# Optimization experiments

Measured on AMD Instinct MI355X. Metric: run time of the kernel, lower is better.

## Reference

```python
import jax, jax.numpy as jnp
import numpy as np

B, P, CD, V = 4096, 64, 2, 3
D, K, H, L, S, NI, NF = 128, 2048, 256, 5, 4, 100000, 10
COMMIT = 0.25
IN_DIM = CD + CD * 2 * NF  # 42


def _lin(k, out, inn):
    kw, kb = jax.random.split(k)
    lim = 1.0 / np.sqrt(inn)
    W = jax.random.uniform(kw, (out, inn), jnp.float32, -lim, lim)
    b = jax.random.uniform(kb, (out,), jnp.float32, -lim, lim)
    return W, b


def setup_inputs() -> dict:
    key = jax.random.key(0)
    ks = jax.random.split(key, 8)
    coords = jax.random.uniform(ks[0], (B, P, CD), jnp.float32) * 2.0 - 1.0
    latent_indices = jax.random.randint(ks[1], (B,), 0, NI)
    latents = jax.random.normal(ks[2], (NI, S, D), jnp.float32)
    emb = jax.random.normal(ks[3], (S, K, D), jnp.float32)
    vq_emb = emb / jnp.linalg.norm(emb, axis=-1, keepdims=True)
    mod = [_lin(jax.random.fold_in(ks[4], i), H, D) for i in range(L)]
    mod_W = jnp.stack([w for w, _ in mod])
    mod_b = jnp.stack([b for _, b in mod])
    dec_W0, dec_b0 = _lin(ks[5], H, IN_DIM)
    hid = [_lin(jax.random.fold_in(ks[6], i), H, H) for i in range(L - 1)]
    dec_Wh = jnp.stack([w for w, _ in hid])
    dec_bh = jnp.stack([b for _, b in hid])
    last_W, last_b = _lin(ks[7], V, H)
    return dict(coords=coords, latent_indices=latent_indices, latents=latents,
                vq_emb=vq_emb, mod_W=mod_W, mod_b=mod_b,
                dec_W0=dec_W0, dec_b0=dec_b0, dec_Wh=dec_Wh, dec_bh=dec_bh,
                last_W=last_W, last_b=last_b)


def reference(coords, latent_indices, latents, vq_emb, mod_W, mod_b,
              dec_W0, dec_b0, dec_Wh, dec_bh, last_W, last_b):
    sg = jax.lax.stop_gradient
    img_lat = latents[latent_indices]  # (B, S, D) gather from large table
    z_q_sum = jnp.zeros((B, D), coords.dtype)
    residual = jnp.zeros((B, D), coords.dtype)
    total_vq_loss = jnp.zeros((), coords.dtype)
    for s in range(S):  # sequential residual VQ stages (structural, S=4)
        z_stage = img_lat[:, s, :]
        if s == 0:
            residual = z_stage
            z_cur = z_stage
        else:
            residual = residual + z_stage
            z_cur = residual - sg(z_q_sum)
        emb = vq_emb[s]  # (K, D)
        # squared distances via expansion: ||z||^2 - 2 z e^T + ||e||^2
        dists = (jnp.sum(z_cur * z_cur, axis=1, keepdims=True)
                 - 2.0 * z_cur @ emb.T
                 + jnp.sum(emb * emb, axis=1))  # (B, K)
        idx = jnp.argmin(dists, axis=1)  # (B,)
        z_q = emb[idx]  # (B, D) codebook gather
        z_q_st = z_cur + sg(z_q - z_cur)  # straight-through
        total_vq_loss = total_vq_loss + COMMIT * jnp.mean((sg(z_q) - z_cur) ** 2)
        z_q_sum = z_q_sum + z_q_st
    # FiLM betas: (L, B, H)
    betas = jnp.einsum('lhd,bd->lbh', mod_W, z_q_sum) + mod_b[:, None, :]
    # positional encoding: concat[x, sin(x*2^f*pi), cos(x*2^f*pi)]
    freqs = (2.0 ** jnp.arange(NF, dtype=coords.dtype)) * np.pi  # (NF,)
    xe = coords[..., None] * freqs  # (B, P, CD, NF)
    enc = jnp.concatenate([coords,
                           jnp.sin(xe).reshape(B, P, -1),
                           jnp.cos(xe).reshape(B, P, -1)], axis=-1)  # (B,P,42)
    x = jax.nn.relu(jnp.einsum('bpi,hi->bph', enc, dec_W0) + dec_b0
                    + betas[0][:, None, :])
    for i in range(1, L):
        x = jax.nn.relu(jnp.einsum('bph,gh->bpg', x, dec_Wh[i - 1]) + dec_bh[i - 1]
                        + betas[i][:, None, :])
    values = jnp.einsum('bph,vh->bpv', x, last_W) + last_b  # (B, P, V)
    return values, total_vq_loss
```

## Files before the change

### kernel.cpp

```cpp
#include <hip/hip_runtime.h>

typedef unsigned short u16;
typedef unsigned int u32;
typedef __attribute__((ext_vector_type(8))) short short8;
typedef __attribute__((ext_vector_type(4))) float f32x4;

__device__ __forceinline__ float b2f(u16 u) {
    return __builtin_bit_cast(float, (u32)u << 16);
}
__device__ __forceinline__ u16 f2b(float f) {
    u32 x = __builtin_bit_cast(u32, f);
    x += 0x7fffu + ((x >> 16) & 1u);
    return (u16)(x >> 16);
}

#define WS_LPART  0
#define WS_ENORM  512
#define WS_ZQSUM  8704
#define WS_BETAS  532992
#define WS_W0PAD  3154432
#define WS_DWH    3162624
#define WS_VQH    WS_BETAS
#define WS_VQL    (WS_BETAS + 524288)

__global__ __launch_bounds__(64) void enorm_kernel(const float* __restrict__ vq,
                                                   float* __restrict__ enorm) {
    int code = blockIdx.x;
    int lane = threadIdx.x;
    const float* e = vq + (size_t)code * 128;
    float a = e[lane], b = e[lane + 64];
    float v = a * a + b * b;
    #pragma unroll
    for (int off = 32; off; off >>= 1) v += __shfl_down(v, off);
    if (lane == 0) enorm[code] = v;
}

__global__ __launch_bounds__(256) void vqsplit_kernel(const float* __restrict__ vq,
                                                      u16* __restrict__ vh,
                                                      u16* __restrict__ vl) {
    int i = blockIdx.x * 256 + threadIdx.x;
    float v = vq[i];
    u16 h = f2b(v);
    vh[i] = h;
    vl[i] = f2b(v - b2f(h));
}

__global__ __launch_bounds__(256) void padw0_kernel(const float* __restrict__ W0,
                                                    u16* __restrict__ w0pad) {
    int i = blockIdx.x * 256 + threadIdx.x;
    int row = i >> 6, k = i & 63;
    w0pad[i] = (k < 42) ? f2b(W0[row * 42 + k]) : (u16)0;
}

__global__ __launch_bounds__(256) void dwh_kernel(const float* __restrict__ Wh,
                                                  u16* __restrict__ dwh) {
    int i = blockIdx.x * 256 + threadIdx.x;
    dwh[i] = f2b(Wh[i]);
}

__global__ __launch_bounds__(512, 2) void vq_kernel(const int* __restrict__ lidx,
                                                    const float* __restrict__ latents,
                                                    const float* __restrict__ vq,
                                                    const u16* __restrict__ vqh,
                                                    const u16* __restrict__ vql,
                                                    const float* __restrict__ enorm,
                                                    float* __restrict__ zqsum_g,
                                                    float* __restrict__ lpartial) {
    int tid = threadIdx.x;
    int wv = tid >> 6;
    int lane = tid & 63;
    int col = lane & 15;
    int g = lane >> 4;
    int urow = tid >> 5;
    int uc = tid & 31;

    __shared__ __align__(16) float s_resid[16][132];
    __shared__ __align__(16) float s_zqsum[16][132];
    __shared__ __align__(16) float s_zcur[16][132];
    __shared__ float rd1[32][16], rd2[32][16];
    __shared__ int   ri1[32][16], ri2[32][16];
    __shared__ int   sel[16];
    __shared__ float lossb[8];

    size_t li_u = (size_t)lidx[blockIdx.x * 16 + urow];

    {
        float4 v = ((const float4*)latents)[li_u * 128 + uc];
        *(float4*)&s_resid[urow][uc * 4] = v;
        *(float4*)&s_zcur[urow][uc * 4]  = v;
        float4 z = {0.f, 0.f, 0.f, 0.f};
        *(float4*)&s_zqsum[urow][uc * 4] = z;
    }
    float loss_local = 0.f;
    __syncthreads();

    for (int s = 0; s < 4; ++s) {
        short8 bh[4], bl[4];
        #pragma unroll
        for (int kc4 = 0; kc4 < 4; ++kc4) {
            int kk = kc4 * 32 + g * 8;
            float4 z0 = *(const float4*)&s_zcur[col][kk];
            float4 z1 = *(const float4*)&s_zcur[col][kk + 4];
            float zz[8] = {z0.x, z0.y, z0.z, z0.w, z1.x, z1.y, z1.z, z1.w};
            short8 h8, l8;
            #pragma unroll
            for (int j = 0; j < 8; ++j) {
                u16 hb = f2b(zz[j]);
                h8[j] = (short)hb;
                l8[j] = (short)f2b(zz[j] - b2f(hb));
            }
            bh[kc4] = h8; bl[kc4] = l8;
        }

        const u16* baseh = vqh + ((size_t)(s * 2048 + wv * 256 + col)) * 128 + g * 8;
        const u16* basel = vql + ((size_t)(s * 2048 + wv * 256 + col)) * 128 + g * 8;
        const float* enb = enorm + s * 2048 + wv * 256 + g * 4;

        float b1 = 3.4e38f, b2v = 3.4e38f; int i1 = 0, i2 = 0;
        auto top2 = [&](float dv, int kv) {
            if (dv < b1)       { b2v = b1; i2 = i1; b1 = dv; i1 = kv; }
            else if (dv < b2v) { b2v = dv; i2 = kv; }
        };

        for (int tp = 0; tp < 8; ++tp) {
            const u16* phA = baseh + (size_t)tp * 32 * 128;
            const u16* plA = basel + (size_t)tp * 32 * 128;
            short8 ahA[4], alA[4], ahB[4], alB[4];
            #pragma unroll
            for (int kc4 = 0; kc4 < 4; ++kc4) {
                ahA[kc4] = *(const short8*)&phA[kc4 * 32];
                alA[kc4] = *(const short8*)&plA[kc4 * 32];
                ahB[kc4] = *(const short8*)&phA[16 * 128 + kc4 * 32];
                alB[kc4] = *(const short8*)&plA[16 * 128 + kc4 * 32];
            }
            f32x4 accA = {0.f, 0.f, 0.f, 0.f};
            f32x4 accB = {0.f, 0.f, 0.f, 0.f};
            #pragma unroll
            for (int kc4 = 0; kc4 < 4; ++kc4) {
                accA = __builtin_amdgcn_mfma_f32_16x16x32_bf16(ahA[kc4], bh[kc4], accA, 0, 0, 0);
                accB = __builtin_amdgcn_mfma_f32_16x16x32_bf16(ahB[kc4], bh[kc4], accB, 0, 0, 0);
                accA = __builtin_amdgcn_mfma_f32_16x16x32_bf16(ahA[kc4], bl[kc4], accA, 0, 0, 0);
                accB = __builtin_amdgcn_mfma_f32_16x16x32_bf16(ahB[kc4], bl[kc4], accB, 0, 0, 0);
                accA = __builtin_amdgcn_mfma_f32_16x16x32_bf16(alA[kc4], bh[kc4], accA, 0, 0, 0);
                accB = __builtin_amdgcn_mfma_f32_16x16x32_bf16(alB[kc4], bh[kc4], accB, 0, 0, 0);
            }
            float4 enA = *(const float4*)&enb[tp * 32];
            float4 enB = *(const float4*)&enb[tp * 32 + 16];
            int kA = wv * 256 + tp * 32 + g * 4;
            int kB = kA + 16;
            top2(enA.x - 2.f * accA[0], kA + 0);
            top2(enA.y - 2.f * accA[1], kA + 1);
            top2(enA.z - 2.f * accA[2], kA + 2);
            top2(enA.w - 2.f * accA[3], kA + 3);
            top2(enB.x - 2.f * accB[0], kB + 0);
            top2(enB.y - 2.f * accB[1], kB + 1);
            top2(enB.z - 2.f * accB[2], kB + 2);
            top2(enB.w - 2.f * accB[3], kB + 3);
        }
        int slot = wv * 4 + g;
        rd1[slot][col] = b1; rd2[slot][col] = b2v;
        ri1[slot][col] = i1; ri2[slot][col] = i2;
        __syncthreads();

        if (tid < 16) {
            float m1 = 3.4e38f, m2 = 3.4e38f; int j1 = 0, j2 = 0;
            for (int sl = 0; sl < 32; ++sl) {
                float d1c = rd1[sl][tid], d2c = rd2[sl][tid];
                int   k1 = ri1[sl][tid], k2 = ri2[sl][tid];
                if (d1c < m1) {
                    float n2; int n2i;
                    if (m1 <= d2c) { n2 = m1; n2i = j1; } else { n2 = d2c; n2i = k2; }
                    m1 = d1c; j1 = k1; m2 = n2; j2 = n2i;
                } else if (d1c < m2) { m2 = d1c; j2 = k1; }
            }
            int jw = j1;
            if (m2 - m1 < 1e-2f) {
                const float* e1p = vq + ((size_t)s * 2048 + j1) * 128;
                const float* e2p = vq + ((size_t)s * 2048 + j2) * 128;
                double t1 = 0.0, t2 = 0.0;
                for (int d = 0; d < 128; ++d) {
                    double z  = (double)s_zcur[tid][d];
                    double e1 = (double)e1p[d], e2 = (double)e2p[d];
                    t1 += e1 * e1 - 2.0 * e1 * z;
                    t2 += e2 * e2 - 2.0 * e2 * z;
                }
                if (t2 < t1 || (t2 == t1 && j2 < j1)) jw = j2;
            }
            sel[tid] = jw;
        }
        __syncthreads();

        {
            int k = sel[urow];
            float4 e = ((const float4*)vq)[((size_t)s * 2048 + k) * 32 + uc];
            int d = uc * 4;
            float4 z4 = *(const float4*)&s_zcur[urow][d];
            float f0 = e.x - z4.x, f1 = e.y - z4.y;
            float f2v = e.z - z4.z, f3 = e.w - z4.w;
            loss_local += f0 * f0 + f1 * f1 + f2v * f2v + f3 * f3;
            float4 zq = *(float4*)&s_zqsum[urow][d];
            zq.x += e.x; zq.y += e.y; zq.z += e.z; zq.w += e.w;
            *(float4*)&s_zqsum[urow][d] = zq;
            if (s < 3) {
                float4 lv = ((const float4*)latents)[li_u * 128 + (size_t)(s + 1) * 32 + uc];
                float4 rs = *(float4*)&s_resid[urow][d];
                rs.x += lv.x; rs.y += lv.y; rs.z += lv.z; rs.w += lv.w;
                *(float4*)&s_resid[urow][d] = rs;
                float4 zcn;
                zcn.x = rs.x - zq.x; zcn.y = rs.y - zq.y;
                zcn.z = rs.z - zq.z; zcn.w = rs.w - zq.w;
                *(float4*)&s_zcur[urow][d] = zcn;
            }
        }
        __syncthreads();
    }

    ((float4*)zqsum_g)[((size_t)blockIdx.x * 16 + urow) * 32 + uc] =
        *(const float4*)&s_zqsum[urow][uc * 4];

    #pragma unroll
    for (int off = 32; off; off >>= 1) loss_local += __shfl_down(loss_local, off);
    if (lane == 0) lossb[wv] = loss_local;
    __syncthreads();
    if (tid == 0) {
        float l = 0.f;
        #pragma unroll
        for (int i = 0; i < 8; ++i) l += lossb[i];
        lpartial[blockIdx.x] = l;
    }
}

__global__ __launch_bounds__(128) void betas_kernel(const float* __restrict__ zqsum,
                                                    const float* __restrict__ mod_W,
                                                    const float* __restrict__ mod_b,
                                                    u16* __restrict__ betas) {
    int bg = blockIdx.x, l = blockIdx.y, t = threadIdx.x;
    __shared__ float zq[16][128];
    for (int u = t; u < 2048; u += 128) ((float*)zq)[u] = zqsum[(size_t)bg * 2048 + u];
    __syncthreads();

    float acc0[16], acc1[16];
    #pragma unroll
    for (int i = 0; i < 16; ++i) { acc0[i] = 0.f; acc1[i] = 0.f; }

    const float4* w0 = (const float4*)(mod_W + ((size_t)l * 256 + t) * 128);
    const float4* w1 = (const float4*)(mod_W + ((size_t)l * 256 + t + 128) * 128);
    #pragma unroll
    for (int c = 0; c < 32; ++c) {
        float4 wa = w0[c], wb = w1[c];
        #pragma unroll
        for (int bb = 0; bb < 16; ++bb) {
            float4 za = *(const float4*)&zq[bb][c * 4];
            acc0[bb] += wa.x * za.x + wa.y * za.y + wa.z * za.z + wa.w * za.w;
            acc1[bb] += wb.x * za.x + wb.y * za.y + wb.z * za.z + wb.w * za.w;
        }
    }
    float bias0 = mod_b[l * 256 + t], bias1 = mod_b[l * 256 + t + 128];
    #pragma unroll
    for (int bb = 0; bb < 16; ++bb) {
        size_t o = ((size_t)l * 4096 + bg * 16 + bb) * 256;
        betas[o + t]       = f2b(acc0[bb] + bias0);
        betas[o + t + 128] = f2b(acc1[bb] + bias1);
    }
}

template<int KD>
__device__ __forceinline__ void gemm_run(const u16* __restrict__ wl, const int wstride,
                                         const u16* __restrict__ xb, const int colsw,
                                         f32x4 acc[4][4]) {
    constexpr int NIT = KD / 32;
    short8 a[2][4], bf[2][4];
    #pragma unroll
    for (int nt = 0; nt < 4; ++nt)
        a[0][nt] = *(const short8*)&wl[(size_t)nt * 16 * wstride];
    #pragma unroll
    for (int mt = 0; mt < 4; ++mt)
        bf[0][mt] = *(const short8*)&xb[mt * 16 * 256 + colsw];
    #pragma unroll
    for (int it = 0; it < NIT; ++it) {
        constexpr int B0 = 0;
        const int cur = it & 1, nxt = cur ^ 1;
        (void)B0;
        if (it + 1 < NIT) {
            const int kc = (it + 1) * 32;
            #pragma unroll
            for (int nt = 0; nt < 4; ++nt)
                a[nxt][nt] = *(const short8*)&wl[(size_t)nt * 16 * wstride + kc];
            #pragma unroll
            for (int mt = 0; mt < 4; ++mt)
                bf[nxt][mt] = *(const short8*)&xb[mt * 16 * 256 + (kc ^ colsw)];
        }
        #pragma unroll
        for (int nt = 0; nt < 4; ++nt)
            #pragma unroll
            for (int mt = 0; mt < 4; ++mt)
                acc[nt][mt] = __builtin_amdgcn_mfma_f32_16x16x32_bf16(
                    a[cur][nt], bf[cur][mt], acc[nt][mt], 0, 0, 0);
    }
}

__global__ __launch_bounds__(256, 3) void mlp_kernel(const float* __restrict__ coords,
                                                     const u16* __restrict__ w0pad,
                                                     const float* __restrict__ dec_b0,
                                                     const u16* __restrict__ dwh,
                                                     const float* __restrict__ dec_bh,
                                                     const float* __restrict__ last_W,
                                                     const float* __restrict__ last_b,
                                                     const u16* __restrict__ betas,
                                                     float* __restrict__ out) {
    __shared__ __align__(16) u16 X[64 * 256];
    int b = blockIdx.x;
    int tid = threadIdx.x;
    int lane = tid & 63, wv = tid >> 6;
    int q = lane >> 4, r16 = lane & 15;
    int nbase = wv * 64;
    int swr = (r16 & 7) << 3;
    int colsw = (q * 8) ^ swr;

    auto xput = [&](int m, int c, u16 val) {
        X[m * 256 + (c ^ ((m & 7) << 3))] = val;
    };

    {
        int m = tid & 63, g = tid >> 6;
        float c0 = coords[((b << 6) + m) * 2 + 0];
        float c1 = coords[((b << 6) + m) * 2 + 1];
        if (g == 0) {
            xput(m, 0, f2b(c0)); xput(m, 1, f2b(c1));
            #pragma unroll
            for (int c = 42; c < 64; ++c) xput(m, c, 0);
            #pragma unroll
            for (int f = 0; f < 10; ++f) {
                float pf = 3.14159265358979323846f * (float)(1 << f);
                xput(m, 32 + f, f2b(cosf(c1 * pf)));
            }
        } else if (g == 1) {
            #pragma unroll
            for (int f = 0; f < 10; ++f) {
                float pf = 3.14159265358979323846f * (float)(1 << f);
                xput(m, 2 + f, f2b(sinf(c0 * pf)));
            }
        } else if (g == 2) {
            #pragma unroll
            for (int f = 0; f < 10; ++f) {
                float pf = 3.14159265358979323846f * (float)(1 << f);
                xput(m, 12 + f, f2b(sinf(c1 * pf)));
            }
        } else {
            #pragma unroll
            for (int f = 0; f < 10; ++f) {
                float pf = 3.14159265358979323846f * (float)(1 << f);
                xput(m, 22 + f, f2b(cosf(c0 * pf)));
            }
        }
    }
    __syncthreads();

    f32x4 acc[4][4];
    const u16* xb = X + r16 * 256;

    auto zero_acc = [&]() {
        #pragma unroll
        for (int nt = 0; nt < 4; ++nt)
            #pragma unroll
            for (int mt = 0; mt < 4; ++mt) {
                f32x4 z = {0.f, 0.f, 0.f, 0.f};
                acc[nt][mt] = z;
            }
    };

    auto epilogue = [&](const float* bias, const u16* beta_l) {
        float bv[4][4];
        #pragma unroll
        for (int nt = 0; nt < 4; ++nt) {
            int n0 = nbase + nt * 16 + q * 4;
            float4 bs = *(const float4*)&bias[n0];
            ushort4 bt = *(const ushort4*)&beta_l[n0];
            bv[nt][0] = bs.x + b2f(bt.x);
            bv[nt][1] = bs.y + b2f(bt.y);
            bv[nt][2] = bs.z + b2f(bt.z);
            bv[nt][3] = bs.w + b2f(bt.w);
        }
        __syncthreads();
        #pragma unroll
        for (int mt = 0; mt < 4; ++mt) {
            int m = mt * 16 + r16;
            #pragma unroll
            for (int nt = 0; nt < 4; ++nt) {
                int n0 = nbase + nt * 16 + q * 4;
                float v0 = fmaxf(acc[nt][mt][0] + bv[nt][0], 0.f);
                float v1 = fmaxf(acc[nt][mt][1] + bv[nt][1], 0.f);
                float v2 = fmaxf(acc[nt][mt][2] + bv[nt][2], 0.f);
                float v3 = fmaxf(acc[nt][mt][3] + bv[nt][3], 0.f);
                uint2 pk;
                pk.x = (u32)f2b(v0) | ((u32)f2b(v1) << 16);
                pk.y = (u32)f2b(v2) | ((u32)f2b(v3) << 16);
                *(uint2*)&X[m * 256 + (n0 ^ swr)] = pk;
            }
        }
        __syncthreads();
    };

    zero_acc();
    gemm_run<64>(w0pad + (size_t)(nbase + r16) * 64 + q * 8, 64, xb, colsw, acc);
    epilogue(dec_b0, betas + (size_t)b * 256);

    #pragma unroll
    for (int l = 1; l < 5; ++l) {
        zero_acc();
        gemm_run<256>(dwh + (size_t)(l - 1) * 65536 + (size_t)(nbase + r16) * 256 + q * 8,
                      256, xb, colsw, acc);
        epilogue(dec_bh + (size_t)(l - 1) * 256, betas + ((size_t)l * 4096 + b) * 256);
    }

    {
        const u16* xt = X + (wv * 16 + r16) * 256;
        const float* lwp = last_W + r16 * 256 + q * 8;
        f32x4 tacc = {0.f, 0.f, 0.f, 0.f};
        #pragma unroll
        for (int kc = 0; kc < 256; kc += 32) {
            short8 xf = *(const short8*)&xt[kc ^ colsw];
            short8 wh, wl8;
            if (r16 < 3) {
                float4 wa = *(const float4*)&lwp[kc];
                float4 wb = *(const float4*)&lwp[kc + 4];
                float ww[8] = {wa.x, wa.y, wa.z, wa.w, wb.x, wb.y, wb.z, wb.w};
                #pragma unroll
                for (int j = 0; j < 8; ++j) {
                    u16 hb = f2b(ww[j]);
                    wh[j]  = (short)hb;
                    wl8[j] = (short)f2b(ww[j] - b2f(hb));
                }
            } else {
                #pragma unroll
                for (int j = 0; j < 8; ++j) { wh[j] = 0; wl8[j] = 0; }
            }
            tacc = __builtin_amdgcn_mfma_f32_16x16x32_bf16(wh,  xf, tacc, 0, 0, 0);
            tacc = __builtin_amdgcn_mfma_f32_16x16x32_bf16(wl8, xf, tacc, 0, 0, 0);
        }
        __syncthreads();
        float* fbuf = (float*)X;
        if (lane < 16) {
            int rr = wv * 16 + lane;
            fbuf[rr * 3 + 0] = tacc[0] + last_b[0];
            fbuf[rr * 3 + 1] = tacc[1] + last_b[1];
            fbuf[rr * 3 + 2] = tacc[2] + last_b[2];
        }
        __syncthreads();
        if (tid < 192) out[(size_t)b * 192 + tid] = fbuf[tid];
    }
}

__global__ __launch_bounds__(64) void finalize_kernel(const float* __restrict__ lpartial,
                                                      float* __restrict__ out) {
    int t = threadIdx.x;
    float s = 0.f;
    for (int i = t; i < 256; i += 64) s += lpartial[i];
    #pragma unroll
    for (int off = 32; off; off >>= 1) s += __shfl_down(s, off);
    if (t == 0) out[786432] = 0.25f * s * (1.f / (4096.f * 128.f));
}

extern "C" void kernel_launch(void* const* d_in, const int* in_sizes, int n_in,
                              void* d_out, int out_size, void* d_ws, size_t ws_size,
                              hipStream_t stream) {
    const float* coords  = (const float*)d_in[0];
    const int*   lidx    = (const int*)d_in[1];
    const float* latents = (const float*)d_in[2];
    const float* vq      = (const float*)d_in[3];
    const float* mod_W   = (const float*)d_in[4];
    const float* mod_b   = (const float*)d_in[5];
    const float* dec_W0  = (const float*)d_in[6];
    const float* dec_b0  = (const float*)d_in[7];
    const float* dec_Wh  = (const float*)d_in[8];
    const float* dec_bh  = (const float*)d_in[9];
    const float* last_W  = (const float*)d_in[10];
    const float* last_b  = (const float*)d_in[11];
    float* out = (float*)d_out;

    float* wsf      = (float*)d_ws;
    float* lpartial = wsf + WS_LPART;
    float* enorm    = wsf + WS_ENORM;
    float* zqsum    = wsf + WS_ZQSUM;
    u16*   betas    = (u16*)(wsf + WS_BETAS);
    u16*   w0pad    = (u16*)(wsf + WS_W0PAD);
    u16*   dwh      = (u16*)(wsf + WS_DWH);
    u16*   vqh      = (u16*)(wsf + WS_VQH);
    u16*   vql      = (u16*)(wsf + WS_VQL);

    enorm_kernel<<<8192, 64, 0, stream>>>(vq, enorm);
    vqsplit_kernel<<<4096, 256, 0, stream>>>(vq, vqh, vql);
    padw0_kernel<<<64, 256, 0, stream>>>(dec_W0, w0pad);
    dwh_kernel<<<1024, 256, 0, stream>>>(dec_Wh, dwh);
    vq_kernel<<<256, 512, 0, stream>>>(lidx, latents, vq, vqh, vql, enorm, zqsum, lpartial);
    betas_kernel<<<dim3(256, 5), 128, 0, stream>>>(zqsum, mod_W, mod_b, betas);
    mlp_kernel<<<4096, 256, 0, stream>>>(coords, w0pad, dec_b0, dwh, dec_bh,
                                         last_W, last_b, betas, out);
    finalize_kernel<<<1, 64, 0, stream>>>(lpartial, out);
}
```

Baseline: 797.0 us.

## Process two images per MLP block, drop register double-buffering, use packed bf16 convert

The MLP kernel now runs 512-thread blocks that each handle two images with separate shared-memory tiles, halving the grid and launching 2048 blocks. The GEMM inner loop drops explicit register double-buffering in favour of simple per-iteration loads, aiming to cut register pressure so the new launch bounds (512 threads, 4 waves per SIMD) can raise occupancy. The epilogue swaps the software round-to-nearest bf16 packing for the hardware v_cvt_pk_bf16_f32 instruction. Risks include doubled LDS per block limiting residency, and less load/compute overlap inside the GEMM.

```diff
diff --git a/kernel.cpp b/kernel.cpp
--- a/kernel.cpp
+++ b/kernel.cpp
@@ -268,38 +268,26 @@
 __device__ __forceinline__ void gemm_run(const u16* __restrict__ wl, const int wstride,
                                          const u16* __restrict__ xb, const int colsw,
                                          f32x4 acc[4][4]) {
-    constexpr int NIT = KD / 32;
-    short8 a[2][4], bf[2][4];
-    #pragma unroll
-    for (int nt = 0; nt < 4; ++nt)
-        a[0][nt] = *(const short8*)&wl[(size_t)nt * 16 * wstride];
-    #pragma unroll
-    for (int mt = 0; mt < 4; ++mt)
-        bf[0][mt] = *(const short8*)&xb[mt * 16 * 256 + colsw];
-    #pragma unroll
-    for (int it = 0; it < NIT; ++it) {
-        constexpr int B0 = 0;
-        const int cur = it & 1, nxt = cur ^ 1;
-        (void)B0;
-        if (it + 1 < NIT) {
-            const int kc = (it + 1) * 32;
-            #pragma unroll
-            for (int nt = 0; nt < 4; ++nt)
-                a[nxt][nt] = *(const short8*)&wl[(size_t)nt * 16 * wstride + kc];
-            #pragma unroll
-            for (int mt = 0; mt < 4; ++mt)
-                bf[nxt][mt] = *(const short8*)&xb[mt * 16 * 256 + (kc ^ colsw)];
-        }
+    #pragma unroll
+    for (int it = 0; it < KD / 32; ++it) {
+        const int kc = it * 32;
+        short8 a[4], bf[4];
+        #pragma unroll
+        for (int nt = 0; nt < 4; ++nt)
+            a[nt] = *(const short8*)&wl[(size_t)nt * 16 * wstride + kc];
+        #pragma unroll
+        for (int mt = 0; mt < 4; ++mt)
+            bf[mt] = *(const short8*)&xb[mt * 16 * 256 + (kc ^ colsw)];
         #pragma unroll
         for (int nt = 0; nt < 4; ++nt)
             #pragma unroll
             for (int mt = 0; mt < 4; ++mt)
                 acc[nt][mt] = __builtin_amdgcn_mfma_f32_16x16x32_bf16(
-                    a[cur][nt], bf[cur][mt], acc[nt][mt], 0, 0, 0);
-    }
-}
-
-__global__ __launch_bounds__(256, 3) void mlp_kernel(const float* __restrict__ coords,
+                    a[nt], bf[mt], acc[nt][mt], 0, 0, 0);
+    }
+}
+
+__global__ __launch_bounds__(512, 4) void mlp_kernel(const float* __restrict__ coords,
                                                      const u16* __restrict__ w0pad,
                                                      const float* __restrict__ dec_b0,
                                                      const u16* __restrict__ dwh,
@@ -308,24 +296,29 @@
                                                      const float* __restrict__ last_b,
                                                      const u16* __restrict__ betas,
                                                      float* __restrict__ out) {
-    __shared__ __align__(16) u16 X[64 * 256];
+    __shared__ __align__(16) u16 X[2 * 64 * 256];
     int b = blockIdx.x;
     int tid = threadIdx.x;
     int lane = tid & 63, wv = tid >> 6;
+    int wv4 = wv & 3, img = wv >> 2;
     int q = lane >> 4, r16 = lane & 15;
-    int nbase = wv * 64;
+    int nbase = wv4 * 64;
     int swr = (r16 & 7) << 3;
     int colsw = (q * 8) ^ swr;
-
-    auto xput = [&](int m, int c, u16 val) {
-        X[m * 256 + (c ^ ((m & 7) << 3))] = val;
-    };
+    int bimg = b * 2 + img;
+    u16* Xi = X + img * 16384;
 
     {
         int m = tid & 63, g = tid >> 6;
-        float c0 = coords[((b << 6) + m) * 2 + 0];
-        float c1 = coords[((b << 6) + m) * 2 + 1];
-        if (g == 0) {
+        int gimg = g >> 2, gg = g & 3;
+        int gbi = b * 2 + gimg;
+        u16* Xg = X + gimg * 16384;
+        auto xput = [&](int mm, int c, u16 val) {
+            Xg[mm * 256 + (c ^ ((mm & 7) << 3))] = val;
+        };
+        float c0 = coords[(((size_t)gbi << 6) + m) * 2 + 0];
+        float c1 = coords[(((size_t)gbi << 6) + m) * 2 + 1];
+        if (gg == 0) {
             xput(m, 0, f2b(c0)); xput(m, 1, f2b(c1));
             #pragma unroll
             for (int c = 42; c < 64; ++c) xput(m, c, 0);
@@ -334,13 +327,13 @@
                 float pf = 3.14159265358979323846f * (float)(1 << f);
                 xput(m, 32 + f, f2b(cosf(c1 * pf)));
             }
-        } else if (g == 1) {
+        } else if (gg == 1) {
             #pragma unroll
             for (int f = 0; f < 10; ++f) {
                 float pf = 3.14159265358979323846f * (float)(1 << f);
                 xput(m, 2 + f, f2b(sinf(c0 * pf)));
             }
-        } else if (g == 2) {
+        } else if (gg == 2) {
             #pragma unroll
             for (int f = 0; f < 10; ++f) {
                 float pf = 3.14159265358979323846f * (float)(1 << f);
@@ -357,7 +350,7 @@
     __syncthreads();
 
     f32x4 acc[4][4];
-    const u16* xb = X + r16 * 256;
+    const u16* xb = Xi + r16 * 256;
 
     auto zero_acc = [&]() {
         #pragma unroll
@@ -393,9 +386,9 @@
                 float v2 = fmaxf(acc[nt][mt][2] + bv[nt][2], 0.f);
                 float v3 = fmaxf(acc[nt][mt][3] + bv[nt][3], 0.f);
                 uint2 pk;
-                pk.x = (u32)f2b(v0) | ((u32)f2b(v1) << 16);
-                pk.y = (u32)f2b(v2) | ((u32)f2b(v3) << 16);
-                *(uint2*)&X[m * 256 + (n0 ^ swr)] = pk;
+                asm("v_cvt_pk_bf16_f32 %0, %1, %2" : "=v"(pk.x) : "v"(v0), "v"(v1));
+                asm("v_cvt_pk_bf16_f32 %0, %1, %2" : "=v"(pk.y) : "v"(v2), "v"(v3));
+                *(uint2*)&Xi[m * 256 + (n0 ^ swr)] = pk;
             }
         }
         __syncthreads();
@@ -403,18 +396,18 @@
 
     zero_acc();
     gemm_run<64>(w0pad + (size_t)(nbase + r16) * 64 + q * 8, 64, xb, colsw, acc);
-    epilogue(dec_b0, betas + (size_t)b * 256);
+    epilogue(dec_b0, betas + (size_t)bimg * 256);
 
     #pragma unroll
     for (int l = 1; l < 5; ++l) {
         zero_acc();
         gemm_run<256>(dwh + (size_t)(l - 1) * 65536 + (size_t)(nbase + r16) * 256 + q * 8,
                       256, xb, colsw, acc);
-        epilogue(dec_bh + (size_t)(l - 1) * 256, betas + ((size_t)l * 4096 + b) * 256);
+        epilogue(dec_bh + (size_t)(l - 1) * 256, betas + ((size_t)l * 4096 + bimg) * 256);
     }
 
     {
-        const u16* xt = X + (wv * 16 + r16) * 256;
+        const u16* xt = Xi + (wv4 * 16 + r16) * 256;
         const float* lwp = last_W + r16 * 256 + q * 8;
         f32x4 tacc = {0.f, 0.f, 0.f, 0.f};
         #pragma unroll
@@ -441,13 +434,13 @@
         __syncthreads();
         float* fbuf = (float*)X;
         if (lane < 16) {
-            int rr = wv * 16 + lane;
-            fbuf[rr * 3 + 0] = tacc[0] + last_b[0];
-            fbuf[rr * 3 + 1] = tacc[1] + last_b[1];
-            fbuf[rr * 3 + 2] = tacc[2] + last_b[2];
-        }
-        __syncthreads();
-        if (tid < 192) out[(size_t)b * 192 + tid] = fbuf[tid];
+            int rr = wv4 * 16 + lane;
+            fbuf[img * 192 + rr * 3 + 0] = tacc[0] + last_b[0];
+            fbuf[img * 192 + rr * 3 + 1] = tacc[1] + last_b[1];
+            fbuf[img * 192 + rr * 3 + 2] = tacc[2] + last_b[2];
+        }
+        __syncthreads();
+        if (tid < 384) out[(size_t)b * 384 + tid] = fbuf[tid];
     }
 }
 
@@ -494,7 +487,7 @@
     dwh_kernel<<<1024, 256, 0, stream>>>(dec_Wh, dwh);
     vq_kernel<<<256, 512, 0, stream>>>(lidx, latents, vq, vqh, vql, enorm, zqsum, lpartial);
     betas_kernel<<<dim3(256, 5), 128, 0, stream>>>(zqsum, mod_W, mod_b, betas);
-    mlp_kernel<<<4096, 256, 0, stream>>>(coords, w0pad, dec_b0, dwh, dec_bh,
+    mlp_kernel<<<2048, 512, 0, stream>>>(coords, w0pad, dec_b0, dwh, dec_bh,
                                          last_W, last_b, betas, out);
     finalize_kernel<<<1, 64, 0, stream>>>(lpartial, out);
 }
```

New measurement: 813.7 us. 2.1% more time.
